# Kernel optimization log

Measured on AMD Instinct MI355X. Metric: run time of the kernel, lower is better.

Reference implementation:

```python
import jax, jax.numpy as jnp
import numpy as np

WARMUP = 5

def _smooth_l1(x):
    a = jnp.abs(x)
    return jnp.where(a < 1.0, 0.5 * a * a, a - 0.5)


def setup_inputs() -> dict:
    key = jax.random.key(0)
    ks = jax.random.split(key, 6)
    B, S, N, M, C = 8, 4, 8192, 50, 10
    return dict(
        pred_boxes=jax.random.normal(ks[0], (B, S, N, 7), jnp.float32),
        pred_classes=jax.random.normal(ks[1], (B, S, N, C), jnp.float32),
        pred_scores=jax.random.normal(ks[2], (B, S, N), jnp.float32),
        gt_boxes=jax.random.normal(ks[3], (B, M, 7), jnp.float32) * 3.0,
        gt_classes=jax.random.randint(ks[4], (B, M), 0, C),
        n_gt=jax.random.randint(ks[5], (B,), 1, M + 1),
        w_center=jnp.float32(2.0),   # loss_weights['center']
        w_obj=jnp.float32(0.5),      # loss_weights['obj']
        w_unmatched=jnp.float32(5.0),# loss_weights['unmatched']
        epoch=0,
    )


def _forward(pred_boxes, pred_classes, pred_scores, gt_boxes, gt_classes, n_gt, w_center, w_obj, w_unmatched, epoch):
    # epoch < WARMUP path: k_factor=10, use_objectness=False, distance_threshold=5.0, cls_weight=0
    K_FACTOR = 10
    COST_THRESH = 5.0 * 10.0  # distance_threshold * 10
    B, S, N, _ = pred_boxes.shape
    M = gt_boxes.shape[1]
    gt_mask = jnp.arange(M)[None, :] < n_gt[:, None]            # [B,M] valid (non-padded) GTs

    pc = pred_boxes[..., :3]                                    # [B,S,N,3]
    gc = gt_boxes[..., :3]                                      # [B,M,3]
    diff = pc[:, :, :, None, :] - gc[:, None, None, :, :]       # [B,S,N,M,3]
    dist = jnp.sqrt(jnp.sum(diff * diff, axis=-1))              # [B,S,N,M] center L2 cost

    # ---- progressive matching (vectorized over B,S,GT) ----
    cost = jnp.where(gt_mask[:, None, None, :], dist, jnp.inf)
    masked = jnp.where(cost < COST_THRESH, cost, jnp.inf)
    neg = -jnp.swapaxes(masked, -1, -2)                         # [B,S,M,N]
    vals, idx = jax.lax.top_k(neg, K_FACTOR)                    # k smallest costs per gt
    pick_ok = vals > -jnp.inf                                   # [B,S,M,k] valid picks
    gt_ids = jnp.broadcast_to(jnp.arange(M, dtype=jnp.int32)[None, None, :, None], idx.shape)
    bidx = jnp.broadcast_to(jnp.arange(B)[:, None, None, None], idx.shape)
    sidx = jnp.broadcast_to(jnp.arange(S)[None, :, None, None], idx.shape)
    assign = jnp.full((B, S, N), -1, dtype=jnp.int32)
    assign = assign.at[bidx, sidx, idx].max(jnp.where(pick_ok, gt_ids, -1))
    matched_gt = pick_ok.any(-1)                                # [B,S,M]
    unmatched = gt_mask[:, None, :] & ~matched_gt               # [B,S,M]

    # ---- center loss (smooth-L1 over matched query/GT center pairs) ----
    pos = assign >= 0                                           # [B,S,N]
    a = jnp.maximum(assign, 0)
    gtc = gc[jnp.arange(B)[:, None, None], a]                   # [B,S,N,3]
    n_pos = pos.sum().astype(jnp.float32)
    loss_center = jnp.sum(_smooth_l1(pc - gtc) * pos[..., None]) / jnp.maximum(n_pos * 3.0, 1.0)

    # ---- progressive objectness loss (BCE-with-logits + dynamic pos_weight) ----
    t = pos.astype(pred_scores.dtype)
    n_neg = jnp.float32(t.size) - n_pos
    pw = jnp.minimum(10.0, n_neg / jnp.maximum(n_pos, 1.0))     # epoch < warmup branch
    x = pred_scores
    loss_obj = jnp.mean(pw * t * jax.nn.softplus(-x) + (1.0 - t) * jax.nn.softplus(x))

    # ---- unmatched-GT loss: pull 5 nearest predictions toward each unmatched GT ----
    dist_t = jnp.swapaxes(dist, -1, -2)                         # [B,S,M,N]
    nd, ni = jax.lax.top_k(-dist_t, 5)
    nd = -nd                                                    # 5 smallest distances [B,S,M,5]
    b5 = jnp.broadcast_to(jnp.arange(B)[:, None, None, None], ni.shape)
    s5 = jnp.broadcast_to(jnp.arange(S)[None, :, None, None], ni.shape)
    obj5 = pred_scores[b5, s5, ni]                              # [B,S,M,5]
    per_gt = jnp.mean(jnp.exp(-nd / 2.0) * (1.0 - obj5), axis=-1)
    per_gt = jnp.where(unmatched, per_gt, 0.0)
    n_entries = jnp.sum(unmatched.any(-1)).astype(jnp.float32)  # number of (b,s) pairs with unmatched gts
    loss_unm = per_gt.sum() / jnp.maximum(n_entries, 1.0)

    return loss_center * w_center + loss_obj * w_obj + loss_unm * w_unmatched


def reference(pred_boxes, pred_classes, pred_scores, gt_boxes, gt_classes, n_gt, w_center, w_obj, w_unmatched, epoch):
    return _forward(pred_boxes, pred_classes, pred_scores, gt_boxes, gt_classes, n_gt, w_center, w_obj, w_unmatched, epoch)
```

## Files before the change

### kernel.cpp

```cpp
#include <hip/hip_runtime.h>

#define NB 8
#define NS 4
#define NN 8192
#define NM 50
#define K10 10
#define COST_THRESH 50.0f
#define LOSS_BLOCKS 256
#define NBUCK 1024
#define NSUB 4
#define CAP 256
#define TOTAL (NB * NS * NN)
#define TT 512
#define ELEMS (NN / TT)

__device__ __forceinline__ bool lexless(float d1, int i1, float d2, int i2) {
  return (d1 < d2) || (d1 == d2 && i1 < i2);
}

__global__ void __launch_bounds__(256) prep_kernel(
    int* __restrict__ assign, float* __restrict__ acc,
    int* __restrict__ bs_unm, int* __restrict__ done) {
  int i = blockIdx.x * blockDim.x + threadIdx.x;
  for (int j = i; j < TOTAL; j += gridDim.x * blockDim.x) assign[j] = -1;
  if (i == 0) { acc[0] = 0.0f; *done = 0; }
  if (i >= 64 && i < 64 + NB * NS) bs_unm[i - 64] = 0;
}

__global__ void __launch_bounds__(TT) topk_kernel(
    const float* __restrict__ pred_boxes, const float* __restrict__ pred_scores,
    const float* __restrict__ gt_boxes, const int* __restrict__ n_gt,
    int* __restrict__ assign, float* __restrict__ per_gt_sum,
    int* __restrict__ bs_unm) {
  const int blk = blockIdx.x;
  const int m = blk % NM;
  const int bs = blk / NM;
  const int b = bs / NS;
  const int t = threadIdx.x;

  __shared__ int shist[NSUB][NBUCK];
  __shared__ float scd[CAP];
  __shared__ int sci[CAP];
  __shared__ float sred[16];
  __shared__ float sbb[2];
  __shared__ int scnt;
  __shared__ int sbucket;
  __shared__ float soutd[K10];
  __shared__ int souti[K10];

  for (int i = t; i < NSUB * NBUCK; i += TT) ((int*)shist)[i] = 0;
  if (t == 0) { scnt = 0; sbucket = NBUCK - 2; }

  const float gx = gt_boxes[(b * NM + m) * 7 + 0];
  const float gy = gt_boxes[(b * NM + m) * 7 + 1];
  const float gz = gt_boxes[(b * NM + m) * 7 + 2];
  const bool valid = (m < n_gt[b]);

  const float* pb = pred_boxes + (size_t)bs * NN * 7;
  float d2r[ELEMS];
  float lmin = INFINITY, lmax = 0.0f;
#pragma unroll
  for (int e = 0; e < ELEMS; e++) {
    int n = t + e * TT;
    float dx = pb[n * 7 + 0] - gx;
    float dy = pb[n * 7 + 1] - gy;
    float dz = pb[n * 7 + 2] - gz;
    float d2 = dx * dx + dy * dy + dz * dz;
    d2r[e] = d2;
    lmin = fminf(lmin, d2);
    lmax = fmaxf(lmax, d2);
  }
#pragma unroll
  for (int off = 32; off >= 1; off >>= 1) {
    lmin = fminf(lmin, __shfl_down(lmin, off));
    lmax = fmaxf(lmax, __shfl_down(lmax, off));
  }
  const int wave = t >> 6;
  if ((t & 63) == 0) { sred[wave] = lmin; sred[8 + wave] = lmax; }
  __syncthreads();
  if (t == 0) {
    float bmin = INFINITY, bmax = 0.0f;
#pragma unroll
    for (int w = 0; w < TT / 64; w++) {
      bmin = fminf(bmin, sred[w]);
      bmax = fmaxf(bmax, sred[8 + w]);
    }
    sbb[0] = bmin;
    sbb[1] = (float)NBUCK / fmaxf(bmax - bmin, 1e-30f);
  }
  __syncthreads();
  const float bmin = sbb[0], scale = sbb[1];

  int* hist = shist[wave & (NSUB - 1)];
#pragma unroll
  for (int e = 0; e < ELEMS; e++) {
    int bidx = (int)((d2r[e] - bmin) * scale);
    bidx = min(NBUCK - 1, max(0, bidx));
    atomicAdd(&hist[bidx], 1);
  }
  __syncthreads();
  for (int i = t; i < NBUCK; i += TT)
    shist[0][i] += shist[1][i] + shist[2][i] + shist[3][i];
  __syncthreads();

  if (t < 64) {
    int lsum = 0;
    for (int i = 0; i < NBUCK / 64; i++) lsum += shist[0][t * (NBUCK / 64) + i];
    int incl = lsum;
#pragma unroll
    for (int off = 1; off < 64; off <<= 1) {
      int v = __shfl_up(incl, off);
      if (t >= off) incl += v;
    }
    int excl = incl - lsum;
    if (excl < K10 && incl >= K10) {
      int c = excl;
      for (int i = 0; i < NBUCK / 64; i++) {
        c += shist[0][t * (NBUCK / 64) + i];
        if (c >= K10) { sbucket = t * (NBUCK / 64) + i; break; }
      }
    }
  }
  __syncthreads();
  const float bound = bmin + ((float)(sbucket + 2) + 0.5f) / scale;

#pragma unroll
  for (int e = 0; e < ELEMS; e++) {
    float d2 = d2r[e];
    if (d2 < bound) {
      int p = atomicAdd(&scnt, 1);
      if (p < CAP) { scd[p] = d2; sci[p] = t + e * TT; }
    }
  }
  __syncthreads();
  const int K = min(scnt, CAP);

  for (int c = t; c < K; c += TT) scd[c] = sqrtf(scd[c]);
  __syncthreads();
  for (int c = t; c < K; c += TT) {
    float dc = scd[c];
    int ic = sci[c];
    int rank = 0;
    for (int o = 0; o < K; o++) rank += lexless(scd[o], sci[o], dc, ic) ? 1 : 0;
    if (rank < K10) { soutd[rank] = dc; souti[rank] = ic; }
  }
  __syncthreads();

  if (t < 64) {
    bool pick = (t < K10) && valid && (soutd[t] < COST_THRESH);
    if (pick) atomicMax(&assign[(size_t)bs * NN + souti[t]], m);
    bool matched = __any(pick);
    if (valid && !matched) {
      float a = 0.0f;
      if (t < 5) a = expf(-0.5f * soutd[t]) * (1.0f - pred_scores[(size_t)bs * NN + souti[t]]);
#pragma unroll
      for (int off = 8; off >= 1; off >>= 1) a += __shfl_down(a, off);
      if (t == 0) {
        atomicAdd(per_gt_sum, a * 0.2f);
        atomicOr(&bs_unm[bs], 1);
      }
    }
  }
}

__global__ void __launch_bounds__(256) loss_final_kernel(
    const float* __restrict__ pred_boxes, const float* __restrict__ pred_scores,
    const float* __restrict__ gt_boxes, const int* __restrict__ assign,
    float* __restrict__ partials, int* __restrict__ done,
    const float* __restrict__ acc, const int* __restrict__ bs_unm,
    const float* __restrict__ wc, const float* __restrict__ wo,
    const float* __restrict__ wu, float* __restrict__ out) {
  int tid = blockIdx.x * blockDim.x + threadIdx.x;
  float lc = 0.0f, spp = 0.0f, spn = 0.0f, np = 0.0f;
  for (int i = tid; i < TOTAL; i += gridDim.x * blockDim.x) {
    int a = assign[i];
    float x = pred_scores[i];
    if (a >= 0) {
      np += 1.0f;
      int b = i / (NS * NN);
      const float* gbp = &gt_boxes[(b * NM + a) * 7];
#pragma unroll
      for (int c = 0; c < 3; c++) {
        float diff = pred_boxes[(size_t)i * 7 + c] - gbp[c];
        float ad = fabsf(diff);
        lc += (ad < 1.0f) ? 0.5f * ad * ad : (ad - 0.5f);
      }
      spp += log1pf(expf(-fabsf(x))) + fmaxf(-x, 0.0f);
    } else {
      spn += log1pf(expf(-fabsf(x))) + fmaxf(x, 0.0f);
    }
  }
#pragma unroll
  for (int off = 32; off >= 1; off >>= 1) {
    lc += __shfl_down(lc, off);
    spp += __shfl_down(spp, off);
    spn += __shfl_down(spn, off);
    np += __shfl_down(np, off);
  }
  __shared__ float red[4][4];
  __shared__ int s_last;
  int wave = threadIdx.x >> 6;
  if ((threadIdx.x & 63) == 0) {
    red[wave][0] = lc; red[wave][1] = spp; red[wave][2] = spn; red[wave][3] = np;
  }
  __syncthreads();
  if (threadIdx.x == 0) {
    float o0 = 0, o1 = 0, o2 = 0, o3 = 0;
#pragma unroll
    for (int w = 0; w < 4; w++) { o0 += red[w][0]; o1 += red[w][1]; o2 += red[w][2]; o3 += red[w][3]; }
    float* p = &partials[(size_t)blockIdx.x * 8];
    __hip_atomic_store(&p[0], o0, __ATOMIC_RELAXED, __HIP_MEMORY_SCOPE_AGENT);
    __hip_atomic_store(&p[1], o1, __ATOMIC_RELAXED, __HIP_MEMORY_SCOPE_AGENT);
    __hip_atomic_store(&p[2], o2, __ATOMIC_RELAXED, __HIP_MEMORY_SCOPE_AGENT);
    __hip_atomic_store(&p[3], o3, __ATOMIC_RELAXED, __HIP_MEMORY_SCOPE_AGENT);
    __threadfence();
    int ticket = __hip_atomic_fetch_add(done, 1, __ATOMIC_ACQ_REL, __HIP_MEMORY_SCOPE_AGENT);
    s_last = (ticket == gridDim.x - 1) ? 1 : 0;
  }
  __syncthreads();
  if (s_last) {
    __threadfence();
    const int t = threadIdx.x;
    float l0 = __hip_atomic_load(&partials[t * 8 + 0], __ATOMIC_RELAXED, __HIP_MEMORY_SCOPE_AGENT);
    float l1 = __hip_atomic_load(&partials[t * 8 + 1], __ATOMIC_RELAXED, __HIP_MEMORY_SCOPE_AGENT);
    float l2 = __hip_atomic_load(&partials[t * 8 + 2], __ATOMIC_RELAXED, __HIP_MEMORY_SCOPE_AGENT);
    float l3 = __hip_atomic_load(&partials[t * 8 + 3], __ATOMIC_RELAXED, __HIP_MEMORY_SCOPE_AGENT);
#pragma unroll
    for (int off = 32; off >= 1; off >>= 1) {
      l0 += __shfl_down(l0, off);
      l1 += __shfl_down(l1, off);
      l2 += __shfl_down(l2, off);
      l3 += __shfl_down(l3, off);
    }
    __shared__ float red2[4][4];
    if ((t & 63) == 0) {
      red2[t >> 6][0] = l0; red2[t >> 6][1] = l1; red2[t >> 6][2] = l2; red2[t >> 6][3] = l3;
    }
    __syncthreads();
    if (t == 0) {
      float o0 = 0, o1 = 0, o2 = 0, o3 = 0;
#pragma unroll
      for (int w = 0; w < 4; w++) { o0 += red2[w][0]; o1 += red2[w][1]; o2 += red2[w][2]; o3 += red2[w][3]; }
      int ne = 0;
      for (int i = 0; i < NB * NS; i++) ne += bs_unm[i];
      float n_pos = o3;
      float loss_center = o0 / fmaxf(n_pos * 3.0f, 1.0f);
      float n_neg = (float)TOTAL - n_pos;
      float pw = fminf(10.0f, n_neg / fmaxf(n_pos, 1.0f));
      float loss_obj = (pw * o1 + o2) / (float)TOTAL;
      float loss_unm = acc[0] / fmaxf((float)ne, 1.0f);
      out[0] = loss_center * wc[0] + loss_obj * wo[0] + loss_unm * wu[0];
    }
  }
}

extern "C" void kernel_launch(void* const* d_in, const int* in_sizes, int n_in,
                              void* d_out, int out_size, void* d_ws, size_t ws_size,
                              hipStream_t stream) {
  const float* pred_boxes = (const float*)d_in[0];
  const float* pred_scores = (const float*)d_in[2];
  const float* gt_boxes = (const float*)d_in[3];
  const int* n_gt = (const int*)d_in[5];
  const float* wc = (const float*)d_in[6];
  const float* wo = (const float*)d_in[7];
  const float* wu = (const float*)d_in[8];
  float* out = (float*)d_out;

  char* ws = (char*)d_ws;
  int* assign = (int*)ws;
  float* acc = (float*)(ws + (size_t)TOTAL * 4);
  int* done = (int*)((char*)acc + 64);
  int* bs_unm = (int*)((char*)acc + 128);
  float* partials = (float*)((char*)acc + 512);

  prep_kernel<<<256, 256, 0, stream>>>(assign, acc, bs_unm, done);
  topk_kernel<<<NB * NS * NM, TT, 0, stream>>>(pred_boxes, pred_scores, gt_boxes,
                                               n_gt, assign, &acc[0], bs_unm);
  loss_final_kernel<<<LOSS_BLOCKS, 256, 0, stream>>>(pred_boxes, pred_scores, gt_boxes, assign,
                                                     partials, done, acc, bs_unm, wc, wo, wu, out);
}
```

Before: 48.21 us.

## Process two ground-truth boxes per top-k block to reuse prediction loads

```diff
diff --git a/kernel.cpp b/kernel.cpp
--- a/kernel.cpp
+++ b/kernel.cpp
@@ -8,7 +8,8 @@
 #define COST_THRESH 50.0f
 #define LOSS_BLOCKS 256
 #define NBUCK 1024
-#define NSUB 4
+#define NSUB 2
+#define MPB 2
 #define CAP 256
 #define TOTAL (NB * NS * NN)
 #define TT 512
@@ -33,129 +34,160 @@
     int* __restrict__ assign, float* __restrict__ per_gt_sum,
     int* __restrict__ bs_unm) {
   const int blk = blockIdx.x;
-  const int m = blk % NM;
-  const int bs = blk / NM;
+  const int mp = blk % (NM / MPB);
+  const int bs = blk / (NM / MPB);
   const int b = bs / NS;
+  const int m0 = mp * MPB;
   const int t = threadIdx.x;
-
-  __shared__ int shist[NSUB][NBUCK];
-  __shared__ float scd[CAP];
-  __shared__ int sci[CAP];
-  __shared__ float sred[16];
-  __shared__ float sbb[2];
-  __shared__ int scnt;
-  __shared__ int sbucket;
-  __shared__ float soutd[K10];
-  __shared__ int souti[K10];
-
-  for (int i = t; i < NSUB * NBUCK; i += TT) ((int*)shist)[i] = 0;
-  if (t == 0) { scnt = 0; sbucket = NBUCK - 2; }
-
-  const float gx = gt_boxes[(b * NM + m) * 7 + 0];
-  const float gy = gt_boxes[(b * NM + m) * 7 + 1];
-  const float gz = gt_boxes[(b * NM + m) * 7 + 2];
-  const bool valid = (m < n_gt[b]);
+  const int wave = t >> 6;
+
+  __shared__ int shist[MPB][NSUB][NBUCK];
+  __shared__ float scd[MPB][CAP];
+  __shared__ int sci[MPB][CAP];
+  __shared__ float sred[4][8];
+  __shared__ float sbb[MPB][2];
+  __shared__ int scnt[MPB];
+  __shared__ int sbucket[MPB];
+  __shared__ float soutd[MPB][K10];
+  __shared__ int souti[MPB][K10];
+
+  for (int i = t; i < MPB * NSUB * NBUCK; i += TT) ((int*)shist)[i] = 0;
+  if (t < MPB) { scnt[t] = 0; sbucket[t] = NBUCK - 2; }
+
+  const float g0x = gt_boxes[(b * NM + m0) * 7 + 0];
+  const float g0y = gt_boxes[(b * NM + m0) * 7 + 1];
+  const float g0z = gt_boxes[(b * NM + m0) * 7 + 2];
+  const float g1x = gt_boxes[(b * NM + m0 + 1) * 7 + 0];
+  const float g1y = gt_boxes[(b * NM + m0 + 1) * 7 + 1];
+  const float g1z = gt_boxes[(b * NM + m0 + 1) * 7 + 2];
+  const int ngt = n_gt[b];
 
   const float* pb = pred_boxes + (size_t)bs * NN * 7;
-  float d2r[ELEMS];
-  float lmin = INFINITY, lmax = 0.0f;
+  float d2a[ELEMS], d2b[ELEMS];
+  float lmin0 = INFINITY, lmax0 = 0.0f, lmin1 = INFINITY, lmax1 = 0.0f;
 #pragma unroll
   for (int e = 0; e < ELEMS; e++) {
     int n = t + e * TT;
-    float dx = pb[n * 7 + 0] - gx;
-    float dy = pb[n * 7 + 1] - gy;
-    float dz = pb[n * 7 + 2] - gz;
+    float x = pb[n * 7 + 0];
+    float y = pb[n * 7 + 1];
+    float z = pb[n * 7 + 2];
+    float dx = x - g0x, dy = y - g0y, dz = z - g0z;
     float d2 = dx * dx + dy * dy + dz * dz;
-    d2r[e] = d2;
-    lmin = fminf(lmin, d2);
-    lmax = fmaxf(lmax, d2);
+    d2a[e] = d2; lmin0 = fminf(lmin0, d2); lmax0 = fmaxf(lmax0, d2);
+    dx = x - g1x; dy = y - g1y; dz = z - g1z;
+    d2 = dx * dx + dy * dy + dz * dz;
+    d2b[e] = d2; lmin1 = fminf(lmin1, d2); lmax1 = fmaxf(lmax1, d2);
   }
 #pragma unroll
   for (int off = 32; off >= 1; off >>= 1) {
-    lmin = fminf(lmin, __shfl_down(lmin, off));
-    lmax = fmaxf(lmax, __shfl_down(lmax, off));
-  }
-  const int wave = t >> 6;
-  if ((t & 63) == 0) { sred[wave] = lmin; sred[8 + wave] = lmax; }
-  __syncthreads();
-  if (t == 0) {
+    lmin0 = fminf(lmin0, __shfl_down(lmin0, off));
+    lmax0 = fmaxf(lmax0, __shfl_down(lmax0, off));
+    lmin1 = fminf(lmin1, __shfl_down(lmin1, off));
+    lmax1 = fmaxf(lmax1, __shfl_down(lmax1, off));
+  }
+  if ((t & 63) == 0) {
+    sred[0][wave] = lmin0; sred[1][wave] = lmax0;
+    sred[2][wave] = lmin1; sred[3][wave] = lmax1;
+  }
+  __syncthreads();
+  if (t < MPB) {
     float bmin = INFINITY, bmax = 0.0f;
 #pragma unroll
     for (int w = 0; w < TT / 64; w++) {
-      bmin = fminf(bmin, sred[w]);
-      bmax = fmaxf(bmax, sred[8 + w]);
-    }
-    sbb[0] = bmin;
-    sbb[1] = (float)NBUCK / fmaxf(bmax - bmin, 1e-30f);
-  }
-  __syncthreads();
-  const float bmin = sbb[0], scale = sbb[1];
-
-  int* hist = shist[wave & (NSUB - 1)];
+      bmin = fminf(bmin, sred[2 * t][w]);
+      bmax = fmaxf(bmax, sred[2 * t + 1][w]);
+    }
+    sbb[t][0] = bmin;
+    sbb[t][1] = (float)NBUCK / fmaxf(bmax - bmin, 1e-30f);
+  }
+  __syncthreads();
+  const float bmin0 = sbb[0][0], scale0 = sbb[0][1];
+  const float bmin1 = sbb[1][0], scale1 = sbb[1][1];
+
+  int* h0 = shist[0][wave & (NSUB - 1)];
+  int* h1 = shist[1][wave & (NSUB - 1)];
 #pragma unroll
   for (int e = 0; e < ELEMS; e++) {
-    int bidx = (int)((d2r[e] - bmin) * scale);
-    bidx = min(NBUCK - 1, max(0, bidx));
-    atomicAdd(&hist[bidx], 1);
-  }
-  __syncthreads();
-  for (int i = t; i < NBUCK; i += TT)
-    shist[0][i] += shist[1][i] + shist[2][i] + shist[3][i];
-  __syncthreads();
-
-  if (t < 64) {
+    int b0 = min(NBUCK - 1, (int)((d2a[e] - bmin0) * scale0));
+    atomicAdd(&h0[b0], 1);
+    int b1 = min(NBUCK - 1, (int)((d2b[e] - bmin1) * scale1));
+    atomicAdd(&h1[b1], 1);
+  }
+  __syncthreads();
+  for (int i = t; i < MPB * NBUCK; i += TT) {
+    int mm = i >> 10, ii = i & (NBUCK - 1);
+    shist[mm][0][ii] += shist[mm][1][ii];
+  }
+  __syncthreads();
+
+  if (t < MPB * 64) {
+    int mw = t >> 6, lane = t & 63;
     int lsum = 0;
-    for (int i = 0; i < NBUCK / 64; i++) lsum += shist[0][t * (NBUCK / 64) + i];
+    for (int i = 0; i < NBUCK / 64; i++) lsum += shist[mw][0][lane * (NBUCK / 64) + i];
     int incl = lsum;
 #pragma unroll
     for (int off = 1; off < 64; off <<= 1) {
       int v = __shfl_up(incl, off);
-      if (t >= off) incl += v;
+      if (lane >= off) incl += v;
     }
     int excl = incl - lsum;
     if (excl < K10 && incl >= K10) {
       int c = excl;
       for (int i = 0; i < NBUCK / 64; i++) {
-        c += shist[0][t * (NBUCK / 64) + i];
-        if (c >= K10) { sbucket = t * (NBUCK / 64) + i; break; }
+        c += shist[mw][0][lane * (NBUCK / 64) + i];
+        if (c >= K10) { sbucket[mw] = lane * (NBUCK / 64) + i; break; }
       }
     }
   }
   __syncthreads();
-  const float bound = bmin + ((float)(sbucket + 2) + 0.5f) / scale;
+  const float bound0 = bmin0 + ((float)(sbucket[0] + 2) + 0.5f) / scale0;
+  const float bound1 = bmin1 + ((float)(sbucket[1] + 2) + 0.5f) / scale1;
 
 #pragma unroll
   for (int e = 0; e < ELEMS; e++) {
-    float d2 = d2r[e];
-    if (d2 < bound) {
-      int p = atomicAdd(&scnt, 1);
-      if (p < CAP) { scd[p] = d2; sci[p] = t + e * TT; }
-    }
-  }
-  __syncthreads();
-  const int K = min(scnt, CAP);
-
-  for (int c = t; c < K; c += TT) scd[c] = sqrtf(scd[c]);
-  __syncthreads();
-  for (int c = t; c < K; c += TT) {
-    float dc = scd[c];
-    int ic = sci[c];
+    if (d2a[e] < bound0) {
+      int p = atomicAdd(&scnt[0], 1);
+      if (p < CAP) { scd[0][p] = d2a[e]; sci[0][p] = t + e * TT; }
+    }
+    if (d2b[e] < bound1) {
+      int p = atomicAdd(&scnt[1], 1);
+      if (p < CAP) { scd[1][p] = d2b[e]; sci[1][p] = t + e * TT; }
+    }
+  }
+  __syncthreads();
+  const int K0 = min(scnt[0], CAP);
+  const int K1 = min(scnt[1], CAP);
+
+  for (int c = t; c < K0; c += TT) scd[0][c] = sqrtf(scd[0][c]);
+  for (int c = t; c < K1; c += TT) scd[1][c] = sqrtf(scd[1][c]);
+  __syncthreads();
+  for (int c = t; c < K0; c += TT) {
+    float dc = scd[0][c]; int ic = sci[0][c];
     int rank = 0;
-    for (int o = 0; o < K; o++) rank += lexless(scd[o], sci[o], dc, ic) ? 1 : 0;
-    if (rank < K10) { soutd[rank] = dc; souti[rank] = ic; }
-  }
-  __syncthreads();
-
-  if (t < 64) {
-    bool pick = (t < K10) && valid && (soutd[t] < COST_THRESH);
-    if (pick) atomicMax(&assign[(size_t)bs * NN + souti[t]], m);
+    for (int o = 0; o < K0; o++) rank += lexless(scd[0][o], sci[0][o], dc, ic) ? 1 : 0;
+    if (rank < K10) { soutd[0][rank] = dc; souti[0][rank] = ic; }
+  }
+  for (int c = t; c < K1; c += TT) {
+    float dc = scd[1][c]; int ic = sci[1][c];
+    int rank = 0;
+    for (int o = 0; o < K1; o++) rank += lexless(scd[1][o], sci[1][o], dc, ic) ? 1 : 0;
+    if (rank < K10) { soutd[1][rank] = dc; souti[1][rank] = ic; }
+  }
+  __syncthreads();
+
+  if (t < MPB * 64) {
+    int mw = t >> 6, lane = t & 63;
+    int m = m0 + mw;
+    bool valid = (m < ngt);
+    bool pick = (lane < K10) && valid && (soutd[mw][lane] < COST_THRESH);
+    if (pick) atomicMax(&assign[(size_t)bs * NN + souti[mw][lane]], m);
     bool matched = __any(pick);
     if (valid && !matched) {
       float a = 0.0f;
-      if (t < 5) a = expf(-0.5f * soutd[t]) * (1.0f - pred_scores[(size_t)bs * NN + souti[t]]);
+      if (lane < 5) a = expf(-0.5f * soutd[mw][lane]) * (1.0f - pred_scores[(size_t)bs * NN + souti[mw][lane]]);
 #pragma unroll
       for (int off = 8; off >= 1; off >>= 1) a += __shfl_down(a, off);
-      if (t == 0) {
+      if (lane == 0) {
         atomicAdd(per_gt_sum, a * 0.2f);
         atomicOr(&bs_unm[bs], 1);
       }
@@ -274,8 +306,8 @@
   float* partials = (float*)((char*)acc + 512);
 
   prep_kernel<<<256, 256, 0, stream>>>(assign, acc, bs_unm, done);
-  topk_kernel<<<NB * NS * NM, TT, 0, stream>>>(pred_boxes, pred_scores, gt_boxes,
-                                               n_gt, assign, &acc[0], bs_unm);
+  topk_kernel<<<NB * NS * (NM / MPB), TT, 0, stream>>>(pred_boxes, pred_scores, gt_boxes,
+                                                       n_gt, assign, &acc[0], bs_unm);
   loss_final_kernel<<<LOSS_BLOCKS, 256, 0, stream>>>(pred_boxes, pred_scores, gt_boxes, assign,
                                                      partials, done, acc, bs_unm, wc, wo, wu, out);
 }
```

Result: no change. 48.83 us (+1.3%).
